# Kernel tuning notes

Measured on AMD Instinct MI355X. Metric: run time of the kernel, lower is better.

Reference implementation:

```python
import jax, jax.numpy as jnp
import numpy as np

D_MODEL = 1024
HEADS = 16
D_HEAD = D_MODEL // HEADS


def setup_inputs() -> dict:
    key = jax.random.key(0)
    ks = jax.random.split(key, 5)
    B, S = 4, 2048
    x = jax.random.normal(ks[0], (B, S, D_MODEL), dtype=jnp.float32)
    # nn.Linear weights are [out, in]; store as [in, out] for x @ W convention
    s_qkv = 1.0 / np.sqrt(D_MODEL)
    w_qkv = jax.random.uniform(ks[1], (D_MODEL, 3 * D_MODEL), jnp.float32, -s_qkv, s_qkv)
    b_qkv = jax.random.uniform(ks[2], (3 * D_MODEL,), jnp.float32, -s_qkv, s_qkv)
    w_proj = jax.random.uniform(ks[3], (D_MODEL, D_MODEL), jnp.float32, -s_qkv, s_qkv)
    b_proj = jax.random.uniform(ks[4], (D_MODEL,), jnp.float32, -s_qkv, s_qkv)
    return {"x": x, "w_qkv": w_qkv, "b_qkv": b_qkv, "w_proj": w_proj, "b_proj": b_proj}


def reference(x, w_qkv, b_qkv, w_proj, b_proj):
    B, S, D = x.shape
    scale = D_HEAD ** (-0.5)
    qkv = x @ w_qkv + b_qkv                        # [B,S,3D]
    qkv = qkv.reshape(B, S, 3, HEADS, D_HEAD)
    qkv = jnp.transpose(qkv, (2, 0, 3, 1, 4))      # [3,B,H,S,dh]
    q, k, v = qkv[0], qkv[1], qkv[2]
    attn = jnp.einsum("bhsd,bhtd->bhst", q, k) * scale
    attn = jax.nn.softmax(attn, axis=-1)
    ctx = jnp.einsum("bhst,bhtd->bhsd", attn, v)   # [B,H,S,dh]
    ctx = jnp.transpose(ctx, (0, 2, 1, 3)).reshape(B, S, D)
    return ctx @ w_proj + b_proj
```

## Files before the change

kernel.cpp:

```cpp
#include <hip/hip_runtime.h>

typedef unsigned short u16;
typedef unsigned int u32;
typedef __attribute__((ext_vector_type(8))) short short8;
typedef __attribute__((ext_vector_type(4))) float f32x4;
typedef __attribute__((ext_vector_type(2))) unsigned int u32x2;

extern "C" __device__ float __ocml_native_exp2_f32(float);

__device__ __forceinline__ u16 f32_to_bf16(float f) {
  u32 u = __builtin_bit_cast(u32, f);
  u += 0x7fffu + ((u >> 16) & 1u);
  return (u16)(u >> 16);
}

__device__ __forceinline__ u32 cvt_pk_bf16(float a, float b) {
  u32 r;
  asm("v_cvt_pk_bf16_f32 %0, %1, %2" : "=v"(r) : "v"(a), "v"(b));
  return r;
}

__device__ __forceinline__ void gload16(const void* g, void* l) {
  __builtin_amdgcn_global_load_lds((const __attribute__((address_space(1))) u32*)g,
                                   (__attribute__((address_space(3))) u32*)l, 16, 0, 0);
}

__global__ __launch_bounds__(256) void cvt_bf16_kernel(const float* __restrict__ in,
                                                       u16* __restrict__ out, int n8) {
  int i = blockIdx.x * 256 + threadIdx.x;
  if (i >= n8) return;
  const float4* p = (const float4*)in + (size_t)i * 2;
  float4 a = p[0], b = p[1];
  int4 v;
  v.x = (int)f32_to_bf16(a.x) | ((int)f32_to_bf16(a.y) << 16);
  v.y = (int)f32_to_bf16(a.z) | ((int)f32_to_bf16(a.w) << 16);
  v.z = (int)f32_to_bf16(b.x) | ((int)f32_to_bf16(b.y) << 16);
  v.w = (int)f32_to_bf16(b.z) | ((int)f32_to_bf16(b.w) << 16);
  *(int4*)(out + (size_t)i * 8) = v;
}

__global__ __launch_bounds__(256) void transpose_bf16_kernel(const float* __restrict__ in,
                                                             u16* __restrict__ out, int R, int C) {
  __shared__ u16 tile[32][33];
  int tx = threadIdx.x & 31, ty = threadIdx.x >> 5;
  int c0 = blockIdx.x * 32, r0 = blockIdx.y * 32;
#pragma unroll
  for (int j = 0; j < 32; j += 8)
    tile[ty + j][tx] = f32_to_bf16(in[(size_t)(r0 + ty + j) * C + c0 + tx]);
  __syncthreads();
#pragma unroll
  for (int j = 0; j < 32; j += 8)
    out[(size_t)(c0 + ty + j) * R + r0 + tx] = tile[tx][ty + j];
}

__global__ __launch_bounds__(512, 2) void gemm256_kernel(
    const u16* __restrict__ A, const u16* __restrict__ Bt, const float* __restrict__ bias,
    u16* __restrict__ qo, u16* __restrict__ ko, u16* __restrict__ vo) {
  __shared__ u16 lds[2][2][2][8192];
  const int tid = threadIdx.x;
  const int lane = tid & 63, w = tid >> 6;
  const int lo = lane & 15, hi = lane >> 4;
  const int wr = w >> 2, wn4 = w & 3;
  const int id = blockIdx.y * gridDim.x + blockIdx.x;
  const int swz = (id & 7) * 48 + (id >> 3);
  const int bn = (swz % 12) * 256, bm = (swz / 12) * 256;
  const int srow4 = lane >> 2;
  const int scol = (lane & 3) ^ ((lane >> 3) & 3);
  const u16* aRow = A + (size_t)(bm + w * 16 + srow4) * 1024 + scol * 8;
  const u16* bRow = Bt + (size_t)(bn + w * 16 + srow4) * 1024 + scol * 8;
  const int achk = (hi ^ ((lo >> 1) & 3)) * 8;
  const int bro = wn4 * 64;

  f32x4 acc[8][4] = {};

#define STG(sdb, sab, shk, tile)                                      \
  if ((tile) < 16) {                                                  \
    const u16* g = ((sab) ? bRow : aRow) + (tile) * 64 + (shk) * 32;  \
    u16* d = &lds[sdb][sab][shk][w * 512];                            \
    gload16(g, d);                                                    \
    gload16(g + 128 * 1024, d + 4096);                                \
  }

#define W8 asm volatile("s_waitcnt vmcnt(8)" ::: "memory")
#define W4 asm volatile("s_waitcnt vmcnt(4)" ::: "memory")
#define W0 asm volatile("s_waitcnt vmcnt(0)" ::: "memory")
#define WN ((void)0)

  STG(0, 0, 0, 0); STG(0, 1, 0, 0); STG(0, 0, 1, 0); STG(0, 1, 1, 0);
  STG(1, 0, 0, 1); STG(1, 1, 0, 1);
  W8;
  __builtin_amdgcn_s_barrier();

#define PHASE(db, MH, KK, sdb, sab, shk, tile, WAITOP)                                           \
  {                                                                                              \
    short8 af[4], bf[4];                                                                         \
    _Pragma("unroll") for (int m4 = 0; m4 < 4; ++m4)                                             \
      af[m4] = *(const short8*)&lds[db][0][KK][(wr * 128 + MH * 64 + m4 * 16 + lo) * 32 + achk]; \
    _Pragma("unroll") for (int ni = 0; ni < 4; ++ni)                                             \
      bf[ni] = *(const short8*)&lds[db][1][KK][(bro + ni * 16 + lo) * 32 + achk];                \
    STG(sdb, sab, shk, tile);                                                                    \
    WAITOP;                                                                                      \
    __builtin_amdgcn_s_barrier();                                                                \
    asm volatile("s_waitcnt lgkmcnt(0)" ::: "memory");                                           \
    __builtin_amdgcn_sched_barrier(0);                                                           \
    __builtin_amdgcn_s_setprio(1);                                                               \
    _Pragma("unroll") for (int m4 = 0; m4 < 4; ++m4)                                             \
      _Pragma("unroll") for (int ni = 0; ni < 4; ++ni)                                           \
        acc[MH * 4 + m4][ni] = __builtin_amdgcn_mfma_f32_16x16x32_bf16(                          \
            af[m4], bf[ni], acc[MH * 4 + m4][ni], 0, 0, 0);                                      \
    __builtin_amdgcn_s_setprio(0);                                                               \
    __builtin_amdgcn_s_barrier();                                                                \
  }

  for (int i = 0; i < 7; ++i) {
    const int t1 = 2 * i + 1, t2 = 2 * i + 2, t3 = 2 * i + 3;
    PHASE(0, 0, 0, 1, 0, 1, t1, WN);
    PHASE(0, 1, 0, 1, 1, 1, t1, W8);
    PHASE(0, 0, 1, 0, 0, 0, t2, WN);
    PHASE(0, 1, 1, 0, 1, 0, t2, W8);
    PHASE(1, 0, 0, 0, 0, 1, t2, WN);
    PHASE(1, 1, 0, 0, 1, 1, t2, W8);
    PHASE(1, 0, 1, 1, 0, 0, t3, WN);
    PHASE(1, 1, 1, 1, 1, 0, t3, W8);
  }
  PHASE(0, 0, 0, 1, 0, 1, 15, WN);
  PHASE(0, 1, 0, 1, 1, 1, 15, W8);
  PHASE(0, 0, 1, 0, 0, 0, 16, WN);
  PHASE(0, 1, 1, 0, 1, 0, 16, W4);
  PHASE(1, 0, 0, 0, 0, 1, 16, WN);
  PHASE(1, 1, 0, 0, 1, 1, 16, W0);
  PHASE(1, 0, 1, 1, 0, 0, 17, WN);
  PHASE(1, 1, 1, 1, 1, 0, 17, WN);
#undef PHASE
#undef STG

  u16* T = &lds[0][0][0][0] + w * 8192;
  const int colbase = bn + wn4 * 64;
  const int part = colbase >> 10;
  const int h = (colbase & 1023) >> 6;
  const int grow0 = bm + wr * 128;
  const int b = grow0 >> 11;
  const int s0 = grow0 & 2047;
  float bv[4];
#pragma unroll
  for (int ni = 0; ni < 4; ++ni) bv[ni] = bias[colbase + ni * 16 + lo];

  if (part < 2) {
#pragma unroll
    for (int mi = 0; mi < 8; ++mi)
#pragma unroll
      for (int ni = 0; ni < 4; ++ni) {
        const int col = ni * 16 + lo;
#pragma unroll
        for (int r = 0; r < 4; ++r) {
          const int row = mi * 16 + hi * 4 + r;
          T[row * 64 + (((col >> 3) ^ (row & 7)) * 8) + (col & 7)] =
              f32_to_bf16(acc[mi][ni][r] + bv[ni]);
        }
      }
    u16* dst = part ? ko : qo;
#pragma unroll
    for (int rr = 0; rr < 16; ++rr) {
      const int row = rr * 8 + (lane >> 3);
      const int c = lane & 7;
      short8 v = *(const short8*)&T[row * 64 + (((c ^ (row & 7)) * 8))];
      *(short8*)&dst[((size_t)(b * 16 + h) * 2048 + s0 + row) * 64 + c * 8] = v;
    }
  } else {
#pragma unroll
    for (int mi = 0; mi < 8; ++mi)
#pragma unroll
      for (int ni = 0; ni < 4; ++ni) {
        const int d = ni * 16 + lo;
        u32x2 wv;
        wv.x = cvt_pk_bf16(acc[mi][ni][0] + bv[ni], acc[mi][ni][1] + bv[ni]);
        wv.y = cvt_pk_bf16(acc[mi][ni][2] + bv[ni], acc[mi][ni][3] + bv[ni]);
        const int chunk = 2 * mi + (hi >> 1);
        *(u32x2*)&T[d * 128 + ((chunk ^ (d & 15)) * 8) + (hi & 1) * 4] = wv;
      }
#pragma unroll
    for (int rr = 0; rr < 16; ++rr) {
      const int u = rr * 64 + lane;
      const int d = u >> 4, c = u & 15;
      short8 v = *(const short8*)&T[d * 128 + ((c ^ (d & 15)) * 8)];
      *(short8*)&vo[((size_t)(b * 16 + h) * 64 + d) * 2048 + s0 + c * 8] = v;
    }
  }
}

template <int MODE>
__global__ __launch_bounds__(256) void gemm_kernel(
    const u16* __restrict__ A, const u16* __restrict__ Bt, const float* __restrict__ bias,
    float* __restrict__ outf, int M, int N, int K) {
  __shared__ u16 Sm[2][2][4096];
  const int tid = threadIdx.x;
  const int id = blockIdx.y * gridDim.x + blockIdx.x;
  const int nwg = gridDim.x * gridDim.y;
  const int swz = (id & 7) * (nwg >> 3) + (id >> 3);
  const int bn = (swz % gridDim.x) * 128;
  const int bm = (swz / gridDim.x) * 128;
  const int lane = tid & 63, wid = tid >> 6;
  const int lo = lane & 15, hi = lane >> 4;
  const int wm = (wid >> 1) * 64, wn = (wid & 1) * 64;
  const int srow = lane >> 2, schk = lane & 3;
  const u16* as0 = A + (size_t)(bm + wid * 32 + srow) * K + schk * 8;
  const u16* bs0 = Bt + (size_t)(bn + wid * 32 + srow) * K + schk * 8;
  const size_t row16 = (size_t)16 * K;

  f32x4 acc[4][4] = {};
  gload16(as0, &Sm[0][0][wid * 1024]);
  gload16(as0 + row16, &Sm[0][0][wid * 1024 + 512]);
  gload16(bs0, &Sm[0][1][wid * 1024]);
  gload16(bs0 + row16, &Sm[0][1][wid * 1024 + 512]);
  int cur = 0;
  for (int k0 = 0; k0 < K; k0 += 32) {
    __syncthreads();
    if (k0 + 32 < K) {
      int nx = cur ^ 1;
      gload16(as0 + k0 + 32, &Sm[nx][0][wid * 1024]);
      gload16(as0 + k0 + 32 + row16, &Sm[nx][0][wid * 1024 + 512]);
      gload16(bs0 + k0 + 32, &Sm[nx][1][wid * 1024]);
      gload16(bs0 + k0 + 32 + row16, &Sm[nx][1][wid * 1024 + 512]);
    }
    const u16* Al = Sm[cur][0];
    const u16* Bl = Sm[cur][1];
    short8 af[4], bfr[4];
#pragma unroll
    for (int mi = 0; mi < 4; ++mi) af[mi] = *(const short8*)&Al[(wm + mi * 16 + lo) * 32 + hi * 8];
#pragma unroll
    for (int ni = 0; ni < 4; ++ni) bfr[ni] = *(const short8*)&Bl[(wn + ni * 16 + lo) * 32 + hi * 8];
#pragma unroll
    for (int mi = 0; mi < 4; ++mi)
#pragma unroll
      for (int ni = 0; ni < 4; ++ni)
        acc[mi][ni] = __builtin_amdgcn_mfma_f32_16x16x32_bf16(af[mi], bfr[ni], acc[mi][ni], 0, 0, 0);
    cur ^= 1;
  }

#pragma unroll
  for (int mi = 0; mi < 4; ++mi)
#pragma unroll
    for (int ni = 0; ni < 4; ++ni) {
      int col = bn + wn + ni * 16 + lo;
      float bvv = bias[col];
#pragma unroll
      for (int r = 0; r < 4; ++r) {
        int row = bm + wm + mi * 16 + hi * 4 + r;
        outf[(size_t)row * N + col] = acc[mi][ni][r] + bvv;
      }
    }
}

__global__ __launch_bounds__(256, 3) void attn_kernel(const u16* __restrict__ Qg,
                                                      const u16* __restrict__ Kg,
                                                      const u16* __restrict__ Vtg,
                                                      u16* __restrict__ ctx) {
  __shared__ u16 KV[2][2][4096];
  __shared__ u16 Pb[4][2048];
  const int tid = threadIdx.x;
  const int lane = tid & 63, wid = tid >> 6;
  const int lo = lane & 15, hi = lane >> 4;
  const int id = blockIdx.y * gridDim.x + blockIdx.x;
  const int swz = (id & 7) * 128 + (id >> 3);
  const int qb = swz & 15, bh = swz >> 4;
  const u16* Qh = Qg + (size_t)bh * (2048 * 64);
  const u16* Kh = Kg + (size_t)bh * (2048 * 64);
  const u16* Vh = Vtg + (size_t)bh * (64 * 2048);

  short8 qf[2][2];
#pragma unroll
  for (int ni = 0; ni < 2; ++ni)
#pragma unroll
    for (int kk = 0; kk < 2; ++kk)
      qf[ni][kk] = *(const short8*)&Qh[(size_t)(qb * 128 + wid * 32 + ni * 16 + lo) * 64 +
                                       kk * 32 + hi * 8];

  const int srow = lane >> 3;
  const int schk = (lane & 7) ^ srow;
  const u16* ksrc = Kh + (size_t)(wid * 16 + srow) * 64 + schk * 8;
  const u16* vsrc = Vh + (size_t)(wid * 16 + srow) * 2048 + schk * 8;

  const short8 ONES = {0x3F80, 0x3F80, 0x3F80, 0x3F80, 0x3F80, 0x3F80, 0x3F80, 0x3F80};
  f32x4 o[2][4] = {};
  f32x4 lst[2] = {};
  const float C = 0.18033688f;

#define STAGE(buf, kt)                                                     \
  do {                                                                     \
    gload16(ksrc + (size_t)(kt) * 4096, &KV[buf][0][wid * 1024]);          \
    gload16(ksrc + (size_t)(kt) * 4096 + 512, &KV[buf][0][wid * 1024 + 512]); \
    gload16(vsrc + (size_t)(kt) * 64, &KV[buf][1][wid * 1024]);            \
    gload16(vsrc + (size_t)(kt) * 64 + 8 * 2048, &KV[buf][1][wid * 1024 + 512]); \
  } while (0)

  STAGE(0, 0);
  int cur = 0;
  for (int kt = 0; kt < 32; ++kt) {
    __syncthreads();
    if (kt < 31) STAGE(cur ^ 1, kt + 1);
    const u16* Ks = KV[cur][0];
    const u16* Vs = KV[cur][1];

    f32x4 sa[4][2] = {};
#pragma unroll
    for (int kk = 0; kk < 2; ++kk) {
      short8 kf[4];
#pragma unroll
      for (int mi = 0; mi < 4; ++mi)
        kf[mi] = *(const short8*)&Ks[(mi * 16 + lo) * 64 + (((kk * 4 + hi) ^ (lo & 7)) * 8)];
      __builtin_amdgcn_s_setprio(1);
#pragma unroll
      for (int mi = 0; mi < 4; ++mi)
#pragma unroll
        for (int ni = 0; ni < 2; ++ni)
          sa[mi][ni] = __builtin_amdgcn_mfma_f32_16x16x32_bf16(kf[mi], qf[ni][kk], sa[mi][ni], 0, 0, 0);
      __builtin_amdgcn_s_setprio(0);
    }

#pragma unroll
    for (int mi = 0; mi < 4; ++mi)
#pragma unroll
      for (int ni = 0; ni < 2; ++ni)
#pragma unroll
        for (int r = 0; r < 4; ++r)
          sa[mi][ni][r] = __ocml_native_exp2_f32(sa[mi][ni][r] * C);

#pragma unroll
    for (int mi = 0; mi < 4; ++mi)
#pragma unroll
      for (int ni = 0; ni < 2; ++ni) {
        u32x2 wv;
        wv.x = cvt_pk_bf16(sa[mi][ni][0], sa[mi][ni][1]);
        wv.y = cvt_pk_bf16(sa[mi][ni][2], sa[mi][ni][3]);
        *(u32x2*)&Pb[wid][(ni * 16 + lo) * 64 +
                          (((2 * mi + (hi >> 1)) ^ (lo & 7)) * 8) + (hi & 1) * 4] = wv;
      }
    asm volatile("s_waitcnt lgkmcnt(0)" ::: "memory");
    __builtin_amdgcn_sched_barrier(0);

#pragma unroll
    for (int kk2 = 0; kk2 < 2; ++kk2) {
      short8 pf[2], vf[4];
#pragma unroll
      for (int qi = 0; qi < 2; ++qi)
        pf[qi] = *(const short8*)&Pb[wid][(qi * 16 + lo) * 64 +
                                          (((4 * kk2 + hi) ^ (lo & 7)) * 8)];
#pragma unroll
      for (int di = 0; di < 4; ++di)
        vf[di] = *(const short8*)&Vs[(di * 16 + lo) * 64 + (((kk2 * 4 + hi) ^ (lo & 7)) * 8)];
      __builtin_amdgcn_s_setprio(1);
#pragma unroll
      for (int qi = 0; qi < 2; ++qi)
        lst[qi] = __builtin_amdgcn_mfma_f32_16x16x32_bf16(pf[qi], ONES, lst[qi], 0, 0, 0);
#pragma unroll
      for (int qi = 0; qi < 2; ++qi)
#pragma unroll
        for (int di = 0; di < 4; ++di)
          o[qi][di] = __builtin_amdgcn_mfma_f32_16x16x32_bf16(pf[qi], vf[di], o[qi][di], 0, 0, 0);
      __builtin_amdgcn_s_setprio(0);
    }
    cur ^= 1;
  }
#undef STAGE

  int b = bh >> 4, h = bh & 15;
#pragma unroll
  for (int qi = 0; qi < 2; ++qi)
#pragma unroll
    for (int r = 0; r < 4; ++r) {
      float inv = __builtin_amdgcn_rcpf(lst[qi][r]);
      int sr = qb * 128 + wid * 32 + qi * 16 + hi * 4 + r;
      u16* crow = ctx + (size_t)(b * 2048 + sr) * 1024 + h * 64;
#pragma unroll
      for (int di = 0; di < 4; ++di) crow[di * 16 + lo] = f32_to_bf16(o[qi][di][r] * inv);
    }
}

extern "C" void kernel_launch(void* const* d_in, const int* in_sizes, int n_in,
                              void* d_out, int out_size, void* d_ws, size_t ws_size,
                              hipStream_t stream) {
  const float* x      = (const float*)d_in[0];
  const float* w_qkv  = (const float*)d_in[1];
  const float* b_qkv  = (const float*)d_in[2];
  const float* w_proj = (const float*)d_in[3];
  const float* b_proj = (const float*)d_in[4];
  float* out = (float*)d_out;
  char* ws = (char*)d_ws;

  u16* xb     = (u16*)(ws);
  u16* wqkvT  = (u16*)(ws + 16777216);
  u16* wprojT = (u16*)(ws + 23068672);
  u16* Vt     = (u16*)(ws + 25165824);
  u16* Q = (u16*)d_out;
  u16* K = Q + 8388608;

  cvt_bf16_kernel<<<4096, 256, 0, stream>>>(x, xb, 1048576);
  transpose_bf16_kernel<<<dim3(96, 32), 256, 0, stream>>>(w_qkv, wqkvT, 1024, 3072);
  transpose_bf16_kernel<<<dim3(32, 32), 256, 0, stream>>>(w_proj, wprojT, 1024, 1024);
  gemm256_kernel<<<dim3(12, 32), 512, 0, stream>>>(xb, wqkvT, b_qkv, Q, K, Vt);
  attn_kernel<<<dim3(16, 64), 256, 0, stream>>>(Q, K, Vt, xb);
  gemm_kernel<1><<<dim3(8, 64), 256, 0, stream>>>(xb, wprojT, b_proj, out, 8192, 1024, 1024);
}
```

Measured before the change: 275.8 us.

## Merge prep kernels, fold softmax scale into Q, widen attention blocks

The three preprocessing kernels (x cast and two weight transposes) become one launch that dispatches on block index. The softmax scale (log2e/sqrt(dh)) is now applied to Q in the QKV GEMM epilogue, which removes a multiply per score inside attention. The attention kernel moves to 512-thread blocks covering 256 query rows, so each staged K/V tile is shared by twice as many queries and each wave issues half as many loads. In exchange, Q is rounded to bf16 after scaling, and the larger blocks with launch bounds (512, 2) change occupancy and register limits.

```diff
diff --git a/kernel.cpp b/kernel.cpp
--- a/kernel.cpp
+++ b/kernel.cpp
@@ -25,25 +25,39 @@
                                    (__attribute__((address_space(3))) u32*)l, 16, 0, 0);
 }
 
-__global__ __launch_bounds__(256) void cvt_bf16_kernel(const float* __restrict__ in,
-                                                       u16* __restrict__ out, int n8) {
-  int i = blockIdx.x * 256 + threadIdx.x;
-  if (i >= n8) return;
-  const float4* p = (const float4*)in + (size_t)i * 2;
-  float4 a = p[0], b = p[1];
-  int4 v;
-  v.x = (int)f32_to_bf16(a.x) | ((int)f32_to_bf16(a.y) << 16);
-  v.y = (int)f32_to_bf16(a.z) | ((int)f32_to_bf16(a.w) << 16);
-  v.z = (int)f32_to_bf16(b.x) | ((int)f32_to_bf16(b.y) << 16);
-  v.w = (int)f32_to_bf16(b.z) | ((int)f32_to_bf16(b.w) << 16);
-  *(int4*)(out + (size_t)i * 8) = v;
-}
-
-__global__ __launch_bounds__(256) void transpose_bf16_kernel(const float* __restrict__ in,
-                                                             u16* __restrict__ out, int R, int C) {
+__global__ __launch_bounds__(256) void prep_kernel(const float* __restrict__ x,
+                                                   u16* __restrict__ xb,
+                                                   const float* __restrict__ w_qkv,
+                                                   u16* __restrict__ wqkvT,
+                                                   const float* __restrict__ w_proj,
+                                                   u16* __restrict__ wprojT) {
   __shared__ u16 tile[32][33];
-  int tx = threadIdx.x & 31, ty = threadIdx.x >> 5;
-  int c0 = blockIdx.x * 32, r0 = blockIdx.y * 32;
+  const int bid = blockIdx.x, tid = threadIdx.x;
+  if (bid < 4096) {
+    int i = bid * 256 + tid;
+    const float4* p = (const float4*)x + (size_t)i * 2;
+    float4 a = p[0], b = p[1];
+    int4 v;
+    v.x = (int)f32_to_bf16(a.x) | ((int)f32_to_bf16(a.y) << 16);
+    v.y = (int)f32_to_bf16(a.z) | ((int)f32_to_bf16(a.w) << 16);
+    v.z = (int)f32_to_bf16(b.x) | ((int)f32_to_bf16(b.y) << 16);
+    v.w = (int)f32_to_bf16(b.z) | ((int)f32_to_bf16(b.w) << 16);
+    *(int4*)(xb + (size_t)i * 8) = v;
+    return;
+  }
+  const float* in;
+  u16* out;
+  int bx, by, C;
+  if (bid < 7168) {
+    int t = bid - 4096;
+    bx = t % 96; by = t / 96; C = 3072; in = w_qkv; out = wqkvT;
+  } else {
+    int t = bid - 7168;
+    bx = t % 32; by = t / 32; C = 1024; in = w_proj; out = wprojT;
+  }
+  const int R = 1024;
+  int tx = tid & 31, ty = tid >> 5;
+  int c0 = bx * 32, r0 = by * 32;
 #pragma unroll
   for (int j = 0; j < 32; j += 8)
     tile[ty + j][tx] = f32_to_bf16(in[(size_t)(r0 + ty + j) * C + c0 + tx]);
@@ -146,6 +160,7 @@
   for (int ni = 0; ni < 4; ++ni) bv[ni] = bias[colbase + ni * 16 + lo];
 
   if (part < 2) {
+    const float scl = (part == 0) ? 0.18033688f : 1.0f;
 #pragma unroll
     for (int mi = 0; mi < 8; ++mi)
 #pragma unroll
@@ -155,7 +170,7 @@
         for (int r = 0; r < 4; ++r) {
           const int row = mi * 16 + hi * 4 + r;
           T[row * 64 + (((col >> 3) ^ (row & 7)) * 8) + (col & 7)] =
-              f32_to_bf16(acc[mi][ni][r] + bv[ni]);
+              f32_to_bf16((acc[mi][ni][r] + bv[ni]) * scl);
         }
       }
     u16* dst = part ? ko : qo;
@@ -251,18 +266,18 @@
     }
 }
 
-__global__ __launch_bounds__(256, 3) void attn_kernel(const u16* __restrict__ Qg,
+__global__ __launch_bounds__(512, 2) void attn_kernel(const u16* __restrict__ Qg,
                                                       const u16* __restrict__ Kg,
                                                       const u16* __restrict__ Vtg,
                                                       u16* __restrict__ ctx) {
   __shared__ u16 KV[2][2][4096];
-  __shared__ u16 Pb[4][2048];
+  __shared__ u16 Pb[8][2048];
   const int tid = threadIdx.x;
   const int lane = tid & 63, wid = tid >> 6;
   const int lo = lane & 15, hi = lane >> 4;
   const int id = blockIdx.y * gridDim.x + blockIdx.x;
-  const int swz = (id & 7) * 128 + (id >> 3);
-  const int qb = swz & 15, bh = swz >> 4;
+  const int swz = (id & 7) * 64 + (id >> 3);
+  const int qb = swz & 7, bh = swz >> 3;
   const u16* Qh = Qg + (size_t)bh * (2048 * 64);
   const u16* Kh = Kg + (size_t)bh * (2048 * 64);
   const u16* Vh = Vtg + (size_t)bh * (64 * 2048);
@@ -272,25 +287,22 @@
   for (int ni = 0; ni < 2; ++ni)
 #pragma unroll
     for (int kk = 0; kk < 2; ++kk)
-      qf[ni][kk] = *(const short8*)&Qh[(size_t)(qb * 128 + wid * 32 + ni * 16 + lo) * 64 +
+      qf[ni][kk] = *(const short8*)&Qh[(size_t)(qb * 256 + wid * 32 + ni * 16 + lo) * 64 +
                                        kk * 32 + hi * 8];
 
   const int srow = lane >> 3;
   const int schk = (lane & 7) ^ srow;
-  const u16* ksrc = Kh + (size_t)(wid * 16 + srow) * 64 + schk * 8;
-  const u16* vsrc = Vh + (size_t)(wid * 16 + srow) * 2048 + schk * 8;
+  const u16* ksrc = Kh + (size_t)(wid * 8 + srow) * 64 + schk * 8;
+  const u16* vsrc = Vh + (size_t)(wid * 8 + srow) * 2048 + schk * 8;
 
   const short8 ONES = {0x3F80, 0x3F80, 0x3F80, 0x3F80, 0x3F80, 0x3F80, 0x3F80, 0x3F80};
   f32x4 o[2][4] = {};
   f32x4 lst[2] = {};
-  const float C = 0.18033688f;
-
-#define STAGE(buf, kt)                                                     \
-  do {                                                                     \
-    gload16(ksrc + (size_t)(kt) * 4096, &KV[buf][0][wid * 1024]);          \
-    gload16(ksrc + (size_t)(kt) * 4096 + 512, &KV[buf][0][wid * 1024 + 512]); \
-    gload16(vsrc + (size_t)(kt) * 64, &KV[buf][1][wid * 1024]);            \
-    gload16(vsrc + (size_t)(kt) * 64 + 8 * 2048, &KV[buf][1][wid * 1024 + 512]); \
+
+#define STAGE(buf, kt)                                            \
+  do {                                                            \
+    gload16(ksrc + (size_t)(kt) * 4096, &KV[buf][0][wid * 512]);  \
+    gload16(vsrc + (size_t)(kt) * 64, &KV[buf][1][wid * 512]);    \
   } while (0)
 
   STAGE(0, 0);
@@ -323,7 +335,7 @@
       for (int ni = 0; ni < 2; ++ni)
 #pragma unroll
         for (int r = 0; r < 4; ++r)
-          sa[mi][ni][r] = __ocml_native_exp2_f32(sa[mi][ni][r] * C);
+          sa[mi][ni][r] = __ocml_native_exp2_f32(sa[mi][ni][r]);
 
 #pragma unroll
     for (int mi = 0; mi < 4; ++mi)
@@ -369,7 +381,7 @@
 #pragma unroll
     for (int r = 0; r < 4; ++r) {
       float inv = __builtin_amdgcn_rcpf(lst[qi][r]);
-      int sr = qb * 128 + wid * 32 + qi * 16 + hi * 4 + r;
+      int sr = qb * 256 + wid * 32 + qi * 16 + hi * 4 + r;
       u16* crow = ctx + (size_t)(b * 2048 + sr) * 1024 + h * 64;
 #pragma unroll
       for (int di = 0; di < 4; ++di) crow[di * 16 + lo] = f32_to_bf16(o[qi][di][r] * inv);
@@ -394,10 +406,8 @@
   u16* Q = (u16*)d_out;
   u16* K = Q + 8388608;
 
-  cvt_bf16_kernel<<<4096, 256, 0, stream>>>(x, xb, 1048576);
-  transpose_bf16_kernel<<<dim3(96, 32), 256, 0, stream>>>(w_qkv, wqkvT, 1024, 3072);
-  transpose_bf16_kernel<<<dim3(32, 32), 256, 0, stream>>>(w_proj, wprojT, 1024, 1024);
+  prep_kernel<<<8192, 256, 0, stream>>>(x, xb, w_qkv, wqkvT, w_proj, wprojT);
   gemm256_kernel<<<dim3(12, 32), 512, 0, stream>>>(xb, wqkvT, b_qkv, Q, K, Vt);
-  attn_kernel<<<dim3(16, 64), 256, 0, stream>>>(Q, K, Vt, xb);
+  attn_kernel<<<dim3(8, 64), 512, 0, stream>>>(Q, K, Vt, xb);
   gemm_kernel<1><<<dim3(8, 64), 256, 0, stream>>>(xb, wprojT, b_proj, out, 8192, 1024, 1024);
 }
```

Result: faster. 252.0 us (-8.6%).
